# Kernel tuning notes

Hardware: AMD Instinct MI355X
Metric: run time of the kernel (lower is better)

## Reference

```python
import jax, jax.numpy as jnp
import numpy as np

N_NODES = 512
STATE_DIM = 32
MESSAGE_DIM = 32
H_MSG = 64
H_RO = 64
N_STEPS = 5


def setup_inputs() -> dict:
    key = jax.random.key(0)
    ks = jax.random.split(key, 20)
    s = 0.01  # torch init: normal(0, 0.01) weights, zero biases
    d, m = STATE_DIM, MESSAGE_DIM
    inp = {
        "J": jax.random.normal(ks[0], (N_NODES, N_NODES), jnp.float32),
        "b": jax.random.normal(ks[1], (N_NODES,), jnp.float32),
        # message-passing MLP
        "mp_W1": jax.random.normal(ks[2], (H_MSG, 2 * d + 3), jnp.float32) * s,
        "mp_b1": jnp.zeros((H_MSG,), jnp.float32),
        "mp_W2": jax.random.normal(ks[3], (H_MSG, H_MSG), jnp.float32) * s,
        "mp_b2": jnp.zeros((H_MSG,), jnp.float32),
        "mp_W3": jax.random.normal(ks[4], (m, H_MSG), jnp.float32) * s,
        "mp_b3": jnp.zeros((m,), jnp.float32),
        # GRU (input = state_dim + message_dim, hidden = state_dim); gate order r,z,n
        "gru_Wih": jax.random.normal(ks[5], (3 * d, d + m), jnp.float32) * 0.1,
        "gru_Whh": jax.random.normal(ks[6], (3 * d, d), jnp.float32) * 0.1,
        "gru_bih": jax.random.normal(ks[7], (3 * d,), jnp.float32) * 0.1,
        "gru_bhh": jax.random.normal(ks[8], (3 * d,), jnp.float32) * 0.1,
        # readout MLP
        "r_W1": jax.random.normal(ks[9], (H_RO, d), jnp.float32) * s,
        "r_b1": jnp.zeros((H_RO,), jnp.float32),
        "r_W2": jax.random.normal(ks[10], (H_RO, H_RO), jnp.float32) * s,
        "r_b2": jnp.zeros((H_RO,), jnp.float32),
        "r_W3": jax.random.normal(ks[11], (2, H_RO), jnp.float32) * s,
        "r_b3": jnp.zeros((2,), jnp.float32),
    }
    return inp


def reference(J, b, mp_W1, mp_b1, mp_W2, mp_b2, mp_W3, mp_b3,
              gru_Wih, gru_Whh, gru_bih, gru_bhh,
              r_W1, r_b1, r_W2, r_b2, r_W3, r_b3):
    n = J.shape[0]
    d = gru_Whh.shape[1]
    # split first message-layer weight by input segments to avoid building [n,n,2d+3]
    Wi, Wj = mp_W1[:, :d], mp_W1[:, d:2 * d]          # [H, d]
    wJ, wbi, wbj = mp_W1[:, 2 * d], mp_W1[:, 2 * d + 1], mp_W1[:, 2 * d + 2]  # [H]

    def step(h, _):
        # pre[i, j, :] = W1 @ cat(h_i, h_j, J_ij, b_i, b_j) + b1
        pre = ((h @ Wi.T)[:, None, :] + (h @ Wj.T)[None, :, :]
               + J[:, :, None] * wJ + b[:, None, None] * wbi
               + b[None, :, None] * wbj + mp_b1)          # [n, n, H]
        m1 = jax.nn.relu(pre)
        m2 = jax.nn.relu(m1 @ mp_W2.T + mp_b2)            # [n, n, H]
        msg = jax.nn.relu(m2 @ mp_W3.T + mp_b3)           # [n, n, M]
        msg_sum = msg.sum(axis=0)                         # sum over senders i -> [n, M]
        # GRU cell over all nodes (torch GRU, gate order r,z,n)
        x = jnp.concatenate([h, msg_sum], axis=-1)        # [n, d+M]
        gi = x @ gru_Wih.T + gru_bih                      # [n, 3d]
        gh = h @ gru_Whh.T + gru_bhh                      # [n, 3d]
        i_r, i_z, i_n = jnp.split(gi, 3, axis=-1)
        h_r, h_z, h_n = jnp.split(gh, 3, axis=-1)
        r = jax.nn.sigmoid(i_r + h_r)
        z = jax.nn.sigmoid(i_z + h_z)
        n_g = jnp.tanh(i_n + r * h_n)
        h_new = (1.0 - z) * n_g + z * h
        return h_new, None

    h0 = jnp.zeros((n, d), J.dtype)
    h, _ = jax.lax.scan(step, h0, None, length=N_STEPS)
    y = jax.nn.relu(h @ r_W1.T + r_b1)
    y = jax.nn.relu(y @ r_W2.T + r_b2)
    y = jax.nn.relu(y @ r_W3.T + r_b3)                    # [n, 2]
    return jax.nn.sigmoid(y)
```

## Files before the change

### kernel.cpp

```cpp
#include <hip/hip_runtime.h>
#include <math.h>

#define NN 512
#define SD 32
#define HM 64
#define NB 256
#define NGRP 16

typedef __bf16 bf16x8 __attribute__((ext_vector_type(8)));
typedef float floatx4 __attribute__((ext_vector_type(4)));
typedef unsigned uintx4 __attribute__((ext_vector_type(4)));

#define OFF_M2F   0
#define OFF_HBS   34816
#define OFF_WIH   112640
#define OFF_WHH   137600
#define OFF_BIH   150272
#define OFF_BHH   150656
#define OFF_MSUM  151040
#define OFF_HJP   152064
#define OFF_H     152576
#define OFF_MSG   152832
#define OFF_GI    153088
#define OFF_GH    153856
#define LDS_TOTAL 154624

struct KParams {
    const float *J, *b, *mpW1, *mpb1, *mpW2, *mpb2, *mpW3, *mpb3;
    const float *Wih, *Whh, *bih, *bhh;
    const float *rW1, *rb1, *rW2, *rb2, *rW3, *rb3;
    float *out;
    unsigned *hb0, *hb1;
    unsigned *bar;
};

__device__ __forceinline__ float sigmoidf_(float x) {
    return 1.0f / (1.0f + __expf(-x));
}

__device__ __forceinline__ unsigned ld_bypass_u32(const unsigned* p) {
    unsigned r;
    asm volatile("global_load_dword %0, %1, off sc0 sc1\n\ts_waitcnt vmcnt(0)"
                 : "=v"(r) : "v"(p) : "memory");
    return r;
}
__device__ __forceinline__ void issue1(const unsigned* p, uintx4& d) {
    asm volatile("global_load_dwordx4 %0, %1, off sc0 sc1"
                 : "=v"(d) : "v"(p));
}
__device__ __forceinline__ void waitall8(uintx4* c) {
    asm volatile("s_waitcnt vmcnt(0)"
                 : "+v"(c[0]), "+v"(c[1]), "+v"(c[2]), "+v"(c[3]),
                   "+v"(c[4]), "+v"(c[5]), "+v"(c[6]), "+v"(c[7]) :: "memory");
}
__device__ __forceinline__ void unpk(unsigned u, float& lo, float& hi) {
    lo = __uint_as_float(u << 16);
    hi = __uint_as_float(u & 0xffff0000u);
}

__device__ __forceinline__ void xbarrier(unsigned* bar, unsigned round, int bid) {
    __syncthreads();
    if (threadIdx.x == 0) {
        unsigned g = (unsigned)bid >> 4;
        unsigned old = atomicAdd(&bar[g * 16], 1u);
        if (old + 1u == round * NGRP) {
            unsigned r2 = atomicAdd(&bar[256], 1u);
            if (r2 + 1u == round * NGRP) {
                atomicMax(&bar[272], round);
            } else {
                while (ld_bypass_u32(&bar[272]) < round) __builtin_amdgcn_s_sleep(2);
            }
        } else {
            while (ld_bypass_u32(&bar[272]) < round) __builtin_amdgcn_s_sleep(2);
        }
    }
    __syncthreads();
}

__global__ __launch_bounds__(512, 1) void fused_kernel(KParams p)
{
    extern __shared__ __align__(16) char smem[];
    float (*m2f)[16][68] = (float(*)[16][68])(smem + OFF_M2F);
    char*  hbS  = smem + OFF_HBS;
    float* WihS = (float*)(smem + OFF_WIH);
    float* WhhS = (float*)(smem + OFF_WHH);
    float* biS  = (float*)(smem + OFF_BIH);
    float* bhS  = (float*)(smem + OFF_BHH);
    float (*msum)[32] = (float(*)[32])(smem + OFF_MSUM);
    float (*hjpS)[64] = (float(*)[64])(smem + OFF_HJP);
    float (*hS)[32]   = (float(*)[32])(smem + OFF_H);
    float (*msgS)[32] = (float(*)[32])(smem + OFF_MSG);
    float (*giS)[96]  = (float(*)[96])(smem + OFF_GI);
    float (*ghS)[96]  = (float(*)[96])(smem + OFF_GH);

    const int tid  = threadIdx.x;
    const int lane = tid & 63;
    const int wave = tid >> 6;
    const int nsel = wave >> 2;
    const int nw   = wave & 3;
    const int j    = blockIdx.x * 2 + nsel;
    const int q    = lane >> 4;
    const int c    = lane & 15;

    for (int n = tid; n < 96 * 64; n += 512)
        WihS[(n >> 6) * 65 + (n & 63)] = p.Wih[n];
    for (int n = tid; n < 96 * 32; n += 512)
        WhhS[(n >> 5) * 33 + (n & 31)] = p.Whh[n];
    if (tid < 96) biS[tid] = p.bih[tid];
    else if (tid < 192) bhS[tid - 96] = p.bhh[tid - 96];

    if (tid < 128) {
        int node = tid >> 6, cc = tid & 63;
        int jj = blockIdx.x * 2 + node;
        const float* wr = p.mpW1 + cc * 67;
        float bj = p.b[jj];
        hjpS[node][cc] = bj * wr[66] + p.mpb1[cc];
        float si = bj * wr[65];
        float sp = __shfl(si, lane ^ 1);
        if (!(lane & 1)) {
            unsigned pk = (unsigned)__builtin_bit_cast(unsigned short, (__bf16)si)
                        | ((unsigned)__builtin_bit_cast(unsigned short, (__bf16)sp) << 16);
            atomicExch(&p.hb0[jj * 32 + (cc >> 1)], pk);
        }
    }

    float wj_r[16], b2v[4], b3v[2];
    #pragma unroll
    for (int s = 0; s < 8; ++s) {
        wj_r[s]     = p.mpW1[(q * 8 + s) * 67 + 64];
        wj_r[8 + s] = p.mpW1[(q * 8 + s + 32) * 67 + 64];
    }
    #pragma unroll
    for (int t4 = 0; t4 < 4; ++t4) b2v[t4] = p.mpb2[t4 * 16 + c];
    #pragma unroll
    for (int t2 = 0; t2 < 2; ++t2) b3v[t2] = p.mpb3[t2 * 16 + c];

    bf16x8 Bw2[2][4], Bw3[2][2];
    #pragma unroll
    for (int f = 0; f < 2; ++f)
        #pragma unroll
        for (int t4 = 0; t4 < 4; ++t4) {
            const float* src = p.mpW2 + (t4 * 16 + c) * 64 + f * 32 + q * 8;
            bf16x8 v;
            #pragma unroll
            for (int s = 0; s < 8; ++s) v[s] = (__bf16)src[s];
            Bw2[f][t4] = v;
        }
    #pragma unroll
    for (int f = 0; f < 2; ++f)
        #pragma unroll
        for (int t2 = 0; t2 < 2; ++t2) {
            const float* src = p.mpW3 + (t2 * 16 + c) * 64 + f * 32 + q * 8;
            bf16x8 v;
            #pragma unroll
            for (int s = 0; s < 8; ++s) v[s] = (__bf16)src[s];
            Bw3[f][t2] = v;
        }

    const float jA = p.J[(nw * 128 + lane) * NN + j];
    const float jB = p.J[(nw * 128 + 64 + lane) * NN + j];

    const floatx4 zero4 = {0.f, 0.f, 0.f, 0.f};

    xbarrier(p.bar, 1, blockIdx.x);

    for (int t = 0; t < 5; ++t) {
        const unsigned* hb_read = (t & 1) ? p.hb1 : p.hb0;
        unsigned*       hb_next = (t & 1) ? p.hb0 : p.hb1;

        {
            uintx4 ck[8];
            #pragma unroll
            for (int k = 0; k < 8; ++k)
                issue1(hb_read + (k * 512 + tid) * 4, ck[k]);
            waitall8(ck);
            #pragma unroll
            for (int k = 0; k < 8; ++k) {
                int n = k * 512 + tid;
                char* dst = hbS + (n >> 3) * 152 + (n & 7) * 16;
                *(uint2*)dst       = make_uint2(ck[k][0], ck[k][1]);
                *(uint2*)(dst + 8) = make_uint2(ck[k][2], ck[k][3]);
            }
        }
        __syncthreads();

        float hjp_r[16];
        #pragma unroll
        for (int s = 0; s < 8; ++s) {
            hjp_r[s]     = hjpS[nsel][q * 8 + s];
            hjp_r[8 + s] = hjpS[nsel][q * 8 + s + 32];
        }
        float accf[2][4];
        #pragma unroll
        for (int t2 = 0; t2 < 2; ++t2)
            #pragma unroll
            for (int r = 0; r < 4; ++r) accf[t2][r] = 0.0f;

        #pragma unroll
        for (int g = 0; g < 8; ++g) {
            const char* rb = hbS + (nw * 128 + g * 16 + c) * 152;
            uint2 u0 = *(const uint2*)(rb + q * 16);
            uint2 u1 = *(const uint2*)(rb + q * 16 + 8);
            uint2 u2 = *(const uint2*)(rb + 64 + q * 16);
            uint2 u3 = *(const uint2*)(rb + 64 + q * 16 + 8);

            float Jv = __shfl((g < 4) ? jA : jB, (g & 3) * 16 + c);

            float f[16];
            unpk(u0.x, f[0],  f[1]);  unpk(u0.y, f[2],  f[3]);
            unpk(u1.x, f[4],  f[5]);  unpk(u1.y, f[6],  f[7]);
            unpk(u2.x, f[8],  f[9]);  unpk(u2.y, f[10], f[11]);
            unpk(u3.x, f[12], f[13]); unpk(u3.y, f[14], f[15]);

            bf16x8 a0, a1;
            #pragma unroll
            for (int s = 0; s < 8; ++s) {
                float v0 = fmaf(Jv, wj_r[s],     f[s]     + hjp_r[s]);
                float v1 = fmaf(Jv, wj_r[8 + s], f[8 + s] + hjp_r[8 + s]);
                a0[s] = (__bf16)fmaxf(v0, 0.0f);
                a1[s] = (__bf16)fmaxf(v1, 0.0f);
            }

            floatx4 c1[4];
            #pragma unroll
            for (int t4 = 0; t4 < 4; ++t4) {
                c1[t4] = __builtin_amdgcn_mfma_f32_16x16x32_bf16(a0, Bw2[0][t4], zero4, 0, 0, 0);
                c1[t4] = __builtin_amdgcn_mfma_f32_16x16x32_bf16(a1, Bw2[1][t4], c1[t4], 0, 0, 0);
            }

            #pragma unroll
            for (int t4 = 0; t4 < 4; ++t4)
                #pragma unroll
                for (int r = 0; r < 4; ++r)
                    m2f[wave][q * 4 + r][t4 * 16 + c] = fmaxf(c1[t4][r] + b2v[t4], 0.0f);

            asm volatile("s_waitcnt lgkmcnt(0)" ::: "memory");

            float4 ra0 = *(const float4*)&m2f[wave][c][q * 8];
            float4 ra1 = *(const float4*)&m2f[wave][c][q * 8 + 4];
            float4 ra2 = *(const float4*)&m2f[wave][c][q * 8 + 32];
            float4 ra3 = *(const float4*)&m2f[wave][c][q * 8 + 36];

            bf16x8 a2, a3;
            a2[0] = (__bf16)ra0.x; a2[1] = (__bf16)ra0.y; a2[2] = (__bf16)ra0.z; a2[3] = (__bf16)ra0.w;
            a2[4] = (__bf16)ra1.x; a2[5] = (__bf16)ra1.y; a2[6] = (__bf16)ra1.z; a2[7] = (__bf16)ra1.w;
            a3[0] = (__bf16)ra2.x; a3[1] = (__bf16)ra2.y; a3[2] = (__bf16)ra2.z; a3[3] = (__bf16)ra2.w;
            a3[4] = (__bf16)ra3.x; a3[5] = (__bf16)ra3.y; a3[6] = (__bf16)ra3.z; a3[7] = (__bf16)ra3.w;

            floatx4 c2[2];
            #pragma unroll
            for (int t2 = 0; t2 < 2; ++t2) {
                c2[t2] = __builtin_amdgcn_mfma_f32_16x16x32_bf16(a2, Bw3[0][t2], zero4, 0, 0, 0);
                c2[t2] = __builtin_amdgcn_mfma_f32_16x16x32_bf16(a3, Bw3[1][t2], c2[t2], 0, 0, 0);
            }
            #pragma unroll
            for (int t2 = 0; t2 < 2; ++t2)
                #pragma unroll
                for (int r = 0; r < 4; ++r)
                    accf[t2][r] += fmaxf(c2[t2][r] + b3v[t2], 0.0f);

            asm volatile("s_waitcnt lgkmcnt(0)" ::: "memory");
        }

        float s0 = accf[0][0] + accf[0][1] + accf[0][2] + accf[0][3];
        float s1 = accf[1][0] + accf[1][1] + accf[1][2] + accf[1][3];
        s0 += __shfl_xor(s0, 16); s0 += __shfl_xor(s0, 32);
        s1 += __shfl_xor(s1, 16); s1 += __shfl_xor(s1, 32);
        if (lane < 16) {
            msum[wave][c]      = s0;
            msum[wave][16 + c] = s1;
        }
        __syncthreads();

        if (tid < 64) {
            int node = tid >> 5, d = tid & 31;
            msgS[node][d] = msum[node * 4 + 0][d] + msum[node * 4 + 1][d] +
                            msum[node * 4 + 2][d] + msum[node * 4 + 3][d];
        }
        __syncthreads();

        if (tid < 192) {
            int node = tid / 96, r = tid % 96;
            int g = r >> 5, d = r & 31;
            const float* wi = WihS + (g * 32 + d) * 65;
            const float* wh = WhhS + (g * 32 + d) * 33;
            float a  = biS[g * 32 + d];
            float bb = bhS[g * 32 + d];
            if (t > 0) {
                #pragma unroll
                for (int k = 0; k < 32; ++k) {
                    float hv = hS[node][k];
                    a  = fmaf(hv, wi[k], a);
                    bb = fmaf(hv, wh[k], bb);
                }
            }
            #pragma unroll
            for (int k = 0; k < 32; ++k) a = fmaf(msgS[node][k], wi[32 + k], a);
            giS[node][r] = a; ghS[node][r] = bb;
        }
        __syncthreads();

        if (tid < 64) {
            int node = tid >> 5, d = tid & 31;
            float r  = sigmoidf_(giS[node][d] + ghS[node][d]);
            float z  = sigmoidf_(giS[node][32 + d] + ghS[node][32 + d]);
            float ng = tanhf(giS[node][64 + d] + r * ghS[node][64 + d]);
            float hold = (t > 0) ? hS[node][d] : 0.0f;
            hS[node][d] = (1.0f - z) * ng + z * hold;
        }
        __syncthreads();

        if (t < 4) {
            if (tid < 128) {
                int node = tid >> 6, cc = tid & 63;
                int jj = blockIdx.x * 2 + node;
                const float* wr = p.mpW1 + cc * 67;
                float bj = p.b[jj];
                float si = bj * wr[65];
                float sj = bj * wr[66] + p.mpb1[cc];
                #pragma unroll
                for (int d = 0; d < 32; ++d) {
                    float hv = hS[node][d];
                    si = fmaf(hv, wr[d], si);
                    sj = fmaf(hv, wr[32 + d], sj);
                }
                hjpS[node][cc] = sj;
                float sp = __shfl(si, lane ^ 1);
                if (!(lane & 1)) {
                    unsigned pk = (unsigned)__builtin_bit_cast(unsigned short, (__bf16)si)
                                | ((unsigned)__builtin_bit_cast(unsigned short, (__bf16)sp) << 16);
                    atomicExch(&hb_next[jj * 32 + (cc >> 1)], pk);
                }
            }
            xbarrier(p.bar, (unsigned)(t + 2), blockIdx.x);
        } else {
            if (wave < 2) {
                int node = wave;
                int jj = blockIdx.x * 2 + node;
                float y1 = p.rb1[lane];
                #pragma unroll
                for (int k = 0; k < 32; ++k) y1 = fmaf(hS[node][k], p.rW1[lane * 32 + k], y1);
                y1 = fmaxf(y1, 0.0f);
                float y2 = p.rb2[lane];
                #pragma unroll
                for (int k = 0; k < 64; ++k) y2 = fmaf(__shfl(y1, k), p.rW2[lane * 64 + k], y2);
                y2 = fmaxf(y2, 0.0f);
                float y3 = (lane < 2) ? p.rb3[lane] : 0.0f;
                #pragma unroll
                for (int k = 0; k < 64; ++k) {
                    float v = __shfl(y2, k);
                    if (lane < 2) y3 = fmaf(v, p.rW3[lane * 64 + k], y3);
                }
                if (lane < 2) p.out[jj * 2 + lane] = sigmoidf_(y3);
            }
        }
    }
}

extern "C" void kernel_launch(void* const* d_in, const int* in_sizes, int n_in,
                              void* d_out, int out_size, void* d_ws, size_t ws_size,
                              hipStream_t stream)
{
    float* ws = (float*)d_ws;

    KParams p;
    p.J    = (const float*)d_in[0];
    p.b    = (const float*)d_in[1];
    p.mpW1 = (const float*)d_in[2];
    p.mpb1 = (const float*)d_in[3];
    p.mpW2 = (const float*)d_in[4];
    p.mpb2 = (const float*)d_in[5];
    p.mpW3 = (const float*)d_in[6];
    p.mpb3 = (const float*)d_in[7];
    p.Wih  = (const float*)d_in[8];
    p.Whh  = (const float*)d_in[9];
    p.bih  = (const float*)d_in[10];
    p.bhh  = (const float*)d_in[11];
    p.rW1  = (const float*)d_in[12];
    p.rb1  = (const float*)d_in[13];
    p.rW2  = (const float*)d_in[14];
    p.rb2  = (const float*)d_in[15];
    p.rW3  = (const float*)d_in[16];
    p.rb3  = (const float*)d_in[17];
    p.out  = (float*)d_out;

    p.hb0  = (unsigned*)ws;
    p.hb1  = (unsigned*)(ws + 16384);
    p.bar  = (unsigned*)(ws + 32768);

    hipMemsetAsync(p.bar, 0, 4096, stream);

    hipFuncSetAttribute((const void*)fused_kernel,
                        hipFuncAttributeMaxDynamicSharedMemorySize, LDS_TOTAL);
    fused_kernel<<<dim3(NB), dim3(512), LDS_TOTAL, stream>>>(p);
}
```

Measured before the change: 177.5 us.

## Switch edge MLP to fp16 packed math and pipeline state staging

Moves the per-edge first layer to packed fp16 arithmetic (pk_add/pk_fma/pk_max) and the MFMAs from bf16 to fp16. The operands are swapped so weights become the A matrix and biases seed the accumulators, and the layer-2 activations stay in fp16 in LDS. The sender-state load from global is split into four chunks, each overlapped with edge compute on the previous chunk instead of one load, wait and barrier. GRU weights are read straight from global rather than staged in LDS, which cuts LDS use, but fp16 intermediates risk precision or overflow changes.

```diff
diff --git a/kernel.cpp b/kernel.cpp
--- a/kernel.cpp
+++ b/kernel.cpp
@@ -7,23 +7,19 @@
 #define NB 256
 #define NGRP 16
 
-typedef __bf16 bf16x8 __attribute__((ext_vector_type(8)));
+typedef _Float16 f16x8 __attribute__((ext_vector_type(8)));
 typedef float floatx4 __attribute__((ext_vector_type(4)));
 typedef unsigned uintx4 __attribute__((ext_vector_type(4)));
 
-#define OFF_M2F   0
-#define OFF_HBS   34816
-#define OFF_WIH   112640
-#define OFF_WHH   137600
-#define OFF_BIH   150272
-#define OFF_BHH   150656
-#define OFF_MSUM  151040
-#define OFF_HJP   152064
-#define OFF_H     152576
-#define OFF_MSG   152832
-#define OFF_GI    153088
-#define OFF_GH    153856
-#define LDS_TOTAL 154624
+#define OFF_HBS   0
+#define OFF_M2L   73728
+#define OFF_MSUM  92160
+#define OFF_HJP   93184
+#define OFF_H     93696
+#define OFF_MSG   93952
+#define OFF_GI    94208
+#define OFF_GH    94976
+#define LDS_TOTAL 95744
 
 struct KParams {
     const float *J, *b, *mpW1, *mpb1, *mpW2, *mpb2, *mpW3, *mpb3;
@@ -38,24 +34,41 @@
     return 1.0f / (1.0f + __expf(-x));
 }
 
+__device__ __forceinline__ unsigned pkrtz(float a, float b) {
+    unsigned r;
+    asm("v_cvt_pkrtz_f16_f32 %0, %1, %2" : "=v"(r) : "v"(a), "v"(b));
+    return r;
+}
+__device__ __forceinline__ unsigned pk_add(unsigned a, unsigned b) {
+    unsigned r;
+    asm("v_pk_add_f16 %0, %1, %2" : "=v"(r) : "v"(a), "v"(b));
+    return r;
+}
+__device__ __forceinline__ unsigned pk_fma(unsigned a, unsigned b, unsigned c) {
+    unsigned r;
+    asm("v_pk_fma_f16 %0, %1, %2, %3" : "=v"(r) : "v"(a), "v"(b), "v"(c));
+    return r;
+}
+__device__ __forceinline__ unsigned pk_relu(unsigned a) {
+    unsigned r, z = 0u;
+    asm("v_pk_max_f16 %0, %1, %2" : "=v"(r) : "v"(a), "v"(z));
+    return r;
+}
+
 __device__ __forceinline__ unsigned ld_bypass_u32(const unsigned* p) {
     unsigned r;
     asm volatile("global_load_dword %0, %1, off sc0 sc1\n\ts_waitcnt vmcnt(0)"
                  : "=v"(r) : "v"(p) : "memory");
     return r;
 }
-__device__ __forceinline__ void issue1(const unsigned* p, uintx4& d) {
-    asm volatile("global_load_dwordx4 %0, %1, off sc0 sc1"
-                 : "=v"(d) : "v"(p));
-}
-__device__ __forceinline__ void waitall8(uintx4* c) {
-    asm volatile("s_waitcnt vmcnt(0)"
-                 : "+v"(c[0]), "+v"(c[1]), "+v"(c[2]), "+v"(c[3]),
-                   "+v"(c[4]), "+v"(c[5]), "+v"(c[6]), "+v"(c[7]) :: "memory");
-}
-__device__ __forceinline__ void unpk(unsigned u, float& lo, float& hi) {
-    lo = __uint_as_float(u << 16);
-    hi = __uint_as_float(u & 0xffff0000u);
+__device__ __forceinline__ void issue16(const unsigned* p, uintx4& d) {
+    asm volatile("global_load_dwordx4 %0, %1, off sc0 sc1" : "=&v"(d) : "v"(p));
+}
+__device__ __forceinline__ void waitc2(uintx4& a, uintx4& b) {
+    asm volatile("s_waitcnt vmcnt(2)" : "+v"(a), "+v"(b) :: "memory");
+}
+__device__ __forceinline__ void waitc0(uintx4& a, uintx4& b) {
+    asm volatile("s_waitcnt vmcnt(0)" : "+v"(a), "+v"(b) :: "memory");
 }
 
 __device__ __forceinline__ void xbarrier(unsigned* bar, unsigned round, int bid) {
@@ -80,12 +93,7 @@
 __global__ __launch_bounds__(512, 1) void fused_kernel(KParams p)
 {
     extern __shared__ __align__(16) char smem[];
-    float (*m2f)[16][68] = (float(*)[16][68])(smem + OFF_M2F);
-    char*  hbS  = smem + OFF_HBS;
-    float* WihS = (float*)(smem + OFF_WIH);
-    float* WhhS = (float*)(smem + OFF_WHH);
-    float* biS  = (float*)(smem + OFF_BIH);
-    float* bhS  = (float*)(smem + OFF_BHH);
+    char* hbS   = smem + OFF_HBS;
     float (*msum)[32] = (float(*)[32])(smem + OFF_MSUM);
     float (*hjpS)[64] = (float(*)[64])(smem + OFF_HJP);
     float (*hS)[32]   = (float(*)[32])(smem + OFF_H);
@@ -102,12 +110,7 @@
     const int q    = lane >> 4;
     const int c    = lane & 15;
 
-    for (int n = tid; n < 96 * 64; n += 512)
-        WihS[(n >> 6) * 65 + (n & 63)] = p.Wih[n];
-    for (int n = tid; n < 96 * 32; n += 512)
-        WhhS[(n >> 5) * 33 + (n & 31)] = p.Whh[n];
-    if (tid < 96) biS[tid] = p.bih[tid];
-    else if (tid < 192) bhS[tid - 96] = p.bhh[tid - 96];
+    char* m2Lw = smem + OFF_M2L + wave * 2304;
 
     if (tid < 128) {
         int node = tid >> 6, cc = tid & 63;
@@ -117,50 +120,48 @@
         hjpS[node][cc] = bj * wr[66] + p.mpb1[cc];
         float si = bj * wr[65];
         float sp = __shfl(si, lane ^ 1);
-        if (!(lane & 1)) {
-            unsigned pk = (unsigned)__builtin_bit_cast(unsigned short, (__bf16)si)
-                        | ((unsigned)__builtin_bit_cast(unsigned short, (__bf16)sp) << 16);
-            atomicExch(&p.hb0[jj * 32 + (cc >> 1)], pk);
-        }
+        if (!(lane & 1))
+            atomicExch(&p.hb0[jj * 32 + (cc >> 1)], pkrtz(si, sp));
     }
 
-    float wj_r[16], b2v[4], b3v[2];
-    #pragma unroll
-    for (int s = 0; s < 8; ++s) {
-        wj_r[s]     = p.mpW1[(q * 8 + s) * 67 + 64];
-        wj_r[8 + s] = p.mpW1[(q * 8 + s + 32) * 67 + 64];
+    unsigned wj2a[4], wj2b[4];
+    #pragma unroll
+    for (int i = 0; i < 4; ++i) {
+        wj2a[i] = pkrtz(p.mpW1[(q * 8 + 2 * i) * 67 + 64],
+                        p.mpW1[(q * 8 + 2 * i + 1) * 67 + 64]);
+        wj2b[i] = pkrtz(p.mpW1[(q * 8 + 2 * i + 32) * 67 + 64],
+                        p.mpW1[(q * 8 + 2 * i + 33) * 67 + 64]);
     }
-    #pragma unroll
-    for (int t4 = 0; t4 < 4; ++t4) b2v[t4] = p.mpb2[t4 * 16 + c];
-    #pragma unroll
-    for (int t2 = 0; t2 < 2; ++t2) b3v[t2] = p.mpb3[t2 * 16 + c];
-
-    bf16x8 Bw2[2][4], Bw3[2][2];
+    floatx4 b2i[4], b3i[2];
+    #pragma unroll
+    for (int t4 = 0; t4 < 4; ++t4)
+        #pragma unroll
+        for (int r = 0; r < 4; ++r) b2i[t4][r] = p.mpb2[t4 * 16 + q * 4 + r];
+    #pragma unroll
+    for (int t2 = 0; t2 < 2; ++t2)
+        #pragma unroll
+        for (int r = 0; r < 4; ++r) b3i[t2][r] = p.mpb3[t2 * 16 + q * 4 + r];
+
+    f16x8 Aw2[2][4], Aw3[2][2];
     #pragma unroll
     for (int f = 0; f < 2; ++f)
         #pragma unroll
         for (int t4 = 0; t4 < 4; ++t4) {
             const float* src = p.mpW2 + (t4 * 16 + c) * 64 + f * 32 + q * 8;
-            bf16x8 v;
-            #pragma unroll
-            for (int s = 0; s < 8; ++s) v[s] = (__bf16)src[s];
-            Bw2[f][t4] = v;
+            #pragma unroll
+            for (int s = 0; s < 8; ++s) Aw2[f][t4][s] = (_Float16)src[s];
         }
     #pragma unroll
     for (int f = 0; f < 2; ++f)
         #pragma unroll
         for (int t2 = 0; t2 < 2; ++t2) {
             const float* src = p.mpW3 + (t2 * 16 + c) * 64 + f * 32 + q * 8;
-            bf16x8 v;
-            #pragma unroll
-            for (int s = 0; s < 8; ++s) v[s] = (__bf16)src[s];
-            Bw3[f][t2] = v;
-        }
-
-    const float jA = p.J[(nw * 128 + lane) * NN + j];
-    const float jB = p.J[(nw * 128 + 64 + lane) * NN + j];
-
-    const floatx4 zero4 = {0.f, 0.f, 0.f, 0.f};
+            #pragma unroll
+            for (int s = 0; s < 8; ++s) Aw3[f][t2][s] = (_Float16)src[s];
+        }
+
+    const float jA = p.J[((8 * (lane >> 4) + nw) * 16 + (lane & 15)) * NN + j];
+    const float jB = p.J[((8 * (lane >> 4) + 4 + nw) * 16 + (lane & 15)) * NN + j];
 
     xbarrier(p.bar, 1, blockIdx.x);
 
@@ -168,107 +169,101 @@
         const unsigned* hb_read = (t & 1) ? p.hb1 : p.hb0;
         unsigned*       hb_next = (t & 1) ? p.hb0 : p.hb1;
 
-        {
-            uintx4 ck[8];
-            #pragma unroll
-            for (int k = 0; k < 8; ++k)
-                issue1(hb_read + (k * 512 + tid) * 4, ck[k]);
-            waitall8(ck);
-            #pragma unroll
-            for (int k = 0; k < 8; ++k) {
-                int n = k * 512 + tid;
-                char* dst = hbS + (n >> 3) * 152 + (n & 7) * 16;
-                *(uint2*)dst       = make_uint2(ck[k][0], ck[k][1]);
-                *(uint2*)(dst + 8) = make_uint2(ck[k][2], ck[k][3]);
-            }
-        }
-        __syncthreads();
-
-        float hjp_r[16];
-        #pragma unroll
-        for (int s = 0; s < 8; ++s) {
-            hjp_r[s]     = hjpS[nsel][q * 8 + s];
-            hjp_r[8 + s] = hjpS[nsel][q * 8 + s + 32];
-        }
+        unsigned hjp2a[4], hjp2b[4];
+        #pragma unroll
+        for (int i = 0; i < 4; ++i) {
+            hjp2a[i] = pkrtz(hjpS[nsel][q * 8 + 2 * i], hjpS[nsel][q * 8 + 2 * i + 1]);
+            hjp2b[i] = pkrtz(hjpS[nsel][q * 8 + 2 * i + 32], hjpS[nsel][q * 8 + 2 * i + 33]);
+        }
+
         float accf[2][4];
         #pragma unroll
         for (int t2 = 0; t2 < 2; ++t2)
             #pragma unroll
             for (int r = 0; r < 4; ++r) accf[t2][r] = 0.0f;
 
-        #pragma unroll
-        for (int g = 0; g < 8; ++g) {
-            const char* rb = hbS + (nw * 128 + g * 16 + c) * 152;
-            uint2 u0 = *(const uint2*)(rb + q * 16);
-            uint2 u1 = *(const uint2*)(rb + q * 16 + 8);
-            uint2 u2 = *(const uint2*)(rb + 64 + q * 16);
-            uint2 u3 = *(const uint2*)(rb + 64 + q * 16 + 8);
-
-            float Jv = __shfl((g < 4) ? jA : jB, (g & 3) * 16 + c);
-
-            float f[16];
-            unpk(u0.x, f[0],  f[1]);  unpk(u0.y, f[2],  f[3]);
-            unpk(u1.x, f[4],  f[5]);  unpk(u1.y, f[6],  f[7]);
-            unpk(u2.x, f[8],  f[9]);  unpk(u2.y, f[10], f[11]);
-            unpk(u3.x, f[12], f[13]); unpk(u3.y, f[14], f[15]);
-
-            bf16x8 a0, a1;
-            #pragma unroll
-            for (int s = 0; s < 8; ++s) {
-                float v0 = fmaf(Jv, wj_r[s],     f[s]     + hjp_r[s]);
-                float v1 = fmaf(Jv, wj_r[8 + s], f[8 + s] + hjp_r[8 + s]);
-                a0[s] = (__bf16)fmaxf(v0, 0.0f);
-                a1[s] = (__bf16)fmaxf(v1, 0.0f);
-            }
+        uintx4 cr[4][2];
+        const unsigned gbase = (unsigned)((tid >> 2) * 32 + (tid & 3) * 8);
+        const unsigned lbase = (unsigned)((tid >> 2) * 144 + (tid & 3) * 32);
+        #define ISSUE(k)  do { const unsigned* gp = hb_read + (k)*4096 + gbase; \
+                               issue16(gp, cr[k][0]); issue16(gp + 4, cr[k][1]); } while (0)
+        #define WRITE(k)  do { char* dst = hbS + (k)*128*144 + lbase; \
+                               *(uintx4*)dst = cr[k][0]; *(uintx4*)(dst+16) = cr[k][1]; } while (0)
+        ISSUE(0); ISSUE(1);
+        waitc2(cr[0][0], cr[0][1]);
+        WRITE(0);
+        ISSUE(2);
+        __syncthreads();
+
+        auto edge_group = [&](int G, float Jv) {
+            const char* rb = hbS + (G * 16 + c) * 144;
+            uintx4 vlo = *(const uintx4*)(rb + q * 16);
+            uintx4 vhi = *(const uintx4*)(rb + 64 + q * 16);
+            const unsigned Jp = pkrtz(Jv, Jv);
+
+            uintx4 a0u, a1u;
+            #pragma unroll
+            for (int i = 0; i < 4; ++i) {
+                a0u[i] = pk_relu(pk_fma(Jp, wj2a[i], pk_add(vlo[i], hjp2a[i])));
+                a1u[i] = pk_relu(pk_fma(Jp, wj2b[i], pk_add(vhi[i], hjp2b[i])));
+            }
+            f16x8 B0 = __builtin_bit_cast(f16x8, a0u);
+            f16x8 B1 = __builtin_bit_cast(f16x8, a1u);
 
             floatx4 c1[4];
             #pragma unroll
             for (int t4 = 0; t4 < 4; ++t4) {
-                c1[t4] = __builtin_amdgcn_mfma_f32_16x16x32_bf16(a0, Bw2[0][t4], zero4, 0, 0, 0);
-                c1[t4] = __builtin_amdgcn_mfma_f32_16x16x32_bf16(a1, Bw2[1][t4], c1[t4], 0, 0, 0);
-            }
-
-            #pragma unroll
-            for (int t4 = 0; t4 < 4; ++t4)
+                c1[t4] = __builtin_amdgcn_mfma_f32_16x16x32_f16(Aw2[0][t4], B0, b2i[t4], 0, 0, 0);
+                c1[t4] = __builtin_amdgcn_mfma_f32_16x16x32_f16(Aw2[1][t4], B1, c1[t4], 0, 0, 0);
+            }
+            #pragma unroll
+            for (int t4 = 0; t4 < 4; ++t4) {
+                unsigned p0 = pkrtz(fmaxf(c1[t4][0], 0.f), fmaxf(c1[t4][1], 0.f));
+                unsigned p1 = pkrtz(fmaxf(c1[t4][2], 0.f), fmaxf(c1[t4][3], 0.f));
+                *(uint2*)(m2Lw + c * 144 + t4 * 32 + q * 8) = make_uint2(p0, p1);
+            }
+            uintx4 rlo = *(const uintx4*)(m2Lw + c * 144 + q * 16);
+            uintx4 rhi = *(const uintx4*)(m2Lw + c * 144 + 64 + q * 16);
+            f16x8 B2lo = __builtin_bit_cast(f16x8, rlo);
+            f16x8 B2hi = __builtin_bit_cast(f16x8, rhi);
+
+            floatx4 c2[2];
+            #pragma unroll
+            for (int t2 = 0; t2 < 2; ++t2) {
+                c2[t2] = __builtin_amdgcn_mfma_f32_16x16x32_f16(Aw3[0][t2], B2lo, b3i[t2], 0, 0, 0);
+                c2[t2] = __builtin_amdgcn_mfma_f32_16x16x32_f16(Aw3[1][t2], B2hi, c2[t2], 0, 0, 0);
+            }
+            #pragma unroll
+            for (int t2 = 0; t2 < 2; ++t2)
                 #pragma unroll
                 for (int r = 0; r < 4; ++r)
-                    m2f[wave][q * 4 + r][t4 * 16 + c] = fmaxf(c1[t4][r] + b2v[t4], 0.0f);
-
-            asm volatile("s_waitcnt lgkmcnt(0)" ::: "memory");
-
-            float4 ra0 = *(const float4*)&m2f[wave][c][q * 8];
-            float4 ra1 = *(const float4*)&m2f[wave][c][q * 8 + 4];
-            float4 ra2 = *(const float4*)&m2f[wave][c][q * 8 + 32];
-            float4 ra3 = *(const float4*)&m2f[wave][c][q * 8 + 36];
-
-            bf16x8 a2, a3;
-            a2[0] = (__bf16)ra0.x; a2[1] = (__bf16)ra0.y; a2[2] = (__bf16)ra0.z; a2[3] = (__bf16)ra0.w;
-            a2[4] = (__bf16)ra1.x; a2[5] = (__bf16)ra1.y; a2[6] = (__bf16)ra1.z; a2[7] = (__bf16)ra1.w;
-            a3[0] = (__bf16)ra2.x; a3[1] = (__bf16)ra2.y; a3[2] = (__bf16)ra2.z; a3[3] = (__bf16)ra2.w;
-            a3[4] = (__bf16)ra3.x; a3[5] = (__bf16)ra3.y; a3[6] = (__bf16)ra3.z; a3[7] = (__bf16)ra3.w;
-
-            floatx4 c2[2];
-            #pragma unroll
-            for (int t2 = 0; t2 < 2; ++t2) {
-                c2[t2] = __builtin_amdgcn_mfma_f32_16x16x32_bf16(a2, Bw3[0][t2], zero4, 0, 0, 0);
-                c2[t2] = __builtin_amdgcn_mfma_f32_16x16x32_bf16(a3, Bw3[1][t2], c2[t2], 0, 0, 0);
-            }
+                    accf[t2][r] += fmaxf(c2[t2][r], 0.0f);
+        };
+
+        #pragma unroll
+        for (int k = 0; k < 4; ++k) {
+            edge_group(8 * k + nw,     __shfl(jA, k * 16 + c));
+            edge_group(8 * k + 4 + nw, __shfl(jB, k * 16 + c));
+            if (k == 0) { waitc2(cr[1][0], cr[1][1]); WRITE(1); ISSUE(3); __syncthreads(); }
+            else if (k == 1) { waitc2(cr[2][0], cr[2][1]); WRITE(2); __syncthreads(); }
+            else if (k == 2) { waitc0(cr[3][0], cr[3][1]); WRITE(3); __syncthreads(); }
+        }
+        #undef ISSUE
+        #undef WRITE
+
+        #pragma unroll
+        for (int m = 1; m < 16; m <<= 1)
             #pragma unroll
             for (int t2 = 0; t2 < 2; ++t2)
                 #pragma unroll
                 for (int r = 0; r < 4; ++r)
-                    accf[t2][r] += fmaxf(c2[t2][r] + b3v[t2], 0.0f);
-
-            asm volatile("s_waitcnt lgkmcnt(0)" ::: "memory");
-        }
-
-        float s0 = accf[0][0] + accf[0][1] + accf[0][2] + accf[0][3];
-        float s1 = accf[1][0] + accf[1][1] + accf[1][2] + accf[1][3];
-        s0 += __shfl_xor(s0, 16); s0 += __shfl_xor(s0, 32);
-        s1 += __shfl_xor(s1, 16); s1 += __shfl_xor(s1, 32);
-        if (lane < 16) {
-            msum[wave][c]      = s0;
-            msum[wave][16 + c] = s1;
+                    accf[t2][r] += __shfl_xor(accf[t2][r], m);
+        if (c == 0) {
+            #pragma unroll
+            for (int t2 = 0; t2 < 2; ++t2)
+                #pragma unroll
+                for (int r = 0; r < 4; ++r)
+                    msum[wave][t2 * 16 + q * 4 + r] = accf[t2][r];
         }
         __syncthreads();
 
@@ -282,11 +277,11 @@
         if (tid < 192) {
             int node = tid / 96, r = tid % 96;
             int g = r >> 5, d = r & 31;
-            const float* wi = WihS + (g * 32 + d) * 65;
-            const float* wh = WhhS + (g * 32 + d) * 33;
-            float a  = biS[g * 32 + d];
-            float bb = bhS[g * 32 + d];
+            const float* wi = p.Wih + (g * 32 + d) * 64;
+            float a  = p.bih[g * 32 + d];
+            float bb = p.bhh[g * 32 + d];
             if (t > 0) {
+                const float* wh = p.Whh + (g * 32 + d) * 32;
                 #pragma unroll
                 for (int k = 0; k < 32; ++k) {
                     float hv = hS[node][k];
@@ -326,11 +321,8 @@
                 }
                 hjpS[node][cc] = sj;
                 float sp = __shfl(si, lane ^ 1);
-                if (!(lane & 1)) {
-                    unsigned pk = (unsigned)__builtin_bit_cast(unsigned short, (__bf16)si)
-                                | ((unsigned)__builtin_bit_cast(unsigned short, (__bf16)sp) << 16);
-                    atomicExch(&hb_next[jj * 32 + (cc >> 1)], pk);
-                }
+                if (!(lane & 1))
+                    atomicExch(&hb_next[jj * 32 + (cc >> 1)], pkrtz(si, sp));
             }
             xbarrier(p.bar, (unsigned)(t + 2), blockIdx.x);
         } else {
@@ -388,9 +380,9 @@
     p.hb1  = (unsigned*)(ws + 16384);
     p.bar  = (unsigned*)(ws + 32768);
 
-    hipMemsetAsync(p.bar, 0, 4096, stream);
-
-    hipFuncSetAttribute((const void*)fused_kernel,
-                        hipFuncAttributeMaxDynamicSharedMemorySize, LDS_TOTAL);
+    (void)hipMemsetAsync(p.bar, 0, 4096, stream);
+
+    (void)hipFuncSetAttribute((const void*)fused_kernel,
+                              hipFuncAttributeMaxDynamicSharedMemorySize, LDS_TOTAL);
     fused_kernel<<<dim3(NB), dim3(512), LDS_TOTAL, stream>>>(p);
 }
```

After: 174.2 us. Within noise of the previous version (-1.9%).
